# Kernel optimization log

Measured on AMD Instinct MI355X. Metric: run time of the kernel, lower is better.

Reference implementation:

```python
import jax, jax.numpy as jnp
import numpy as np

B, N, C, H = 16, 577, 384, 6
ONE_DIM = 24
RPD = 2 * ONE_DIM - 1  # 47
NUM_CLS = 1
HEAD_DIM = C // H
SCALE = HEAD_DIM ** -0.5


def _build_rel_pos_index():
    # Faithful to the torch loop: tmp[dy - y + off, dx - x + off] with
    # torch's negative-index wraparound -> modulo RPD.
    off = ONE_DIM // 2
    qy = np.repeat(np.arange(ONE_DIM), ONE_DIM)  # (Np,) y of each query patch
    qx = np.tile(np.arange(ONE_DIM), ONE_DIM)    # (Np,) x of each query patch
    ky, kx = qy, qx                              # key patches use same grid
    ry = (ky[None, :] - qy[:, None] + off) % RPD
    rx = (kx[None, :] - qx[:, None] + off) % RPD
    return jnp.asarray(ry * RPD + rx, dtype=jnp.int32)  # (Np, Np)


def setup_inputs() -> dict:
    key = jax.random.key(0)
    k = jax.random.split(key, 6)
    x = jax.random.normal(k[0], (B, N, C), dtype=jnp.float32)
    qkv_w = jax.random.normal(k[1], (3 * C, C), dtype=jnp.float32) * 0.02
    qkv_b = jnp.zeros((3 * C,), dtype=jnp.float32)
    proj_w = jax.random.normal(k[2], (C, C), dtype=jnp.float32) * 0.02
    proj_b = jnp.zeros((C,), dtype=jnp.float32)
    rel_pos = jax.random.normal(k[3], (H, RPD * RPD), dtype=jnp.float32) * 0.02
    mask = jax.random.randint(k[4], (B, N, N), 0, 2, dtype=jnp.int32)
    return {
        "x": x, "qkv_w": qkv_w, "qkv_b": qkv_b,
        "proj_w": proj_w, "proj_b": proj_b, "rel_pos": rel_pos,
        "rel_pos_index": _build_rel_pos_index(),
        "mask": mask, "patch_attn": 1,
    }


def reference(x, qkv_w, qkv_b, proj_w, proj_b, rel_pos, rel_pos_index, mask, patch_attn):
    # qkv projection: torch Linear -> x @ W^T + b
    qkv = x @ qkv_w.T + qkv_b                               # (B, N, 3C)
    qkv = qkv.reshape(B, N, 3, H, HEAD_DIM).transpose(2, 0, 3, 1, 4)
    q, k, v = qkv[0], qkv[1], qkv[2]                        # (B, H, N, hd)

    attn = jnp.einsum("bhqd,bhkd->bhqk", q, k) * SCALE      # (B, H, N, N)

    if patch_attn:
        # gather per-head relative-position bias for patch tokens
        bias = rel_pos[:, rel_pos_index]                    # (H, Np, Np)
        attn = attn.at[:, :, NUM_CLS:, NUM_CLS:].add(bias)

    neg = jnp.finfo(attn.dtype).min
    attn = jnp.where(mask[:, None, :, :] == 0, neg, attn)   # broadcast over heads

    attn = jax.nn.softmax(attn, axis=-1)
    out = jnp.einsum("bhqk,bhkd->bhqd", attn, v)            # (B, H, N, hd)
    out = out.transpose(0, 2, 1, 3).reshape(B, N, C)
    out = out @ proj_w.T + proj_b
    return out
```

## Files before the change

kernel.cpp:

```cpp
#include <hip/hip_runtime.h>
#include <float.h>
#include <math.h>

#define NB 16
#define NN 577
#define NC 384
#define NH 6
#define ND 64
#define RPD2 2209
#define MTOT 9232
#define MPAD 9344
#define SCALE_ 0.125f
#define NEGBIG -3.0e38f
#define BSTRIDE 580
#define NKPAD 640

typedef __attribute__((ext_vector_type(8))) short bf16x8;
typedef __attribute__((ext_vector_type(4))) float f32x4;
typedef unsigned short u16;

#define MFMA16(a, b, c) __builtin_amdgcn_mfma_f32_16x16x32_bf16(a, b, c, 0, 0, 0)

#define SQA 3932160ull
#define OFF_QH 0ull
#define OFF_QL SQA
#define OFF_KH (2ull * SQA)
#define OFF_KL (3ull * SQA)
#define OFF_VTH (4ull * SQA)
#define OFF_VTL (5ull * SQA)
#define OFF_XH (6ull * SQA)
#define OFF_XL (6ull * SQA + 3588096ull)
#define OFF_WQH (6ull * SQA + 2ull * 3588096ull)
#define OFF_WQL (OFF_WQH + 442368ull)
#define OFF_WPH (OFF_WQL + 442368ull)
#define OFF_WPL (OFF_WPH + 147456ull)
#define OFF_BT  (OFF_WPL + 147456ull)
#define OFF_PM  (OFF_BT + 2007960ull)

static __device__ __forceinline__ u16 f2bf(float f) {
  unsigned u = __float_as_uint(f);
  u += 0x7fff + ((u >> 16) & 1);
  return (u16)(u >> 16);
}
static __device__ __forceinline__ float bf2f(u16 h) {
  return __uint_as_float((unsigned)h << 16);
}
static __device__ __forceinline__ void split2(float v, u16& hi, u16& lo) {
  hi = f2bf(v);
  lo = f2bf(v - bf2f(hi));
}
static __device__ __forceinline__ void gload16(const void* g, void* l) {
  __builtin_amdgcn_global_load_lds(
      (const __attribute__((address_space(1))) void*)g,
      (__attribute__((address_space(3))) void*)l, 16, 0, 0);
}

__global__ __launch_bounds__(256) void prep_k(
    const float* __restrict__ x, const float* __restrict__ wq,
    const float* __restrict__ wp, u16* __restrict__ ws)
{
  const int q = blockIdx.x * 256 + threadIdx.x;
  float4 v = {0.f, 0.f, 0.f, 0.f};
  u16 *dh, *dl;
  if (q < 897024) {
    if (q < 886272) v = ((const float4*)x)[q];
    dh = ws + OFF_XH + 4ull * q;
    dl = ws + OFF_XL + 4ull * q;
  } else if (q < 1007616) {
    int t = q - 897024;
    v = ((const float4*)wq)[t];
    dh = ws + OFF_WQH + 4ull * t;
    dl = ws + OFF_WQL + 4ull * t;
  } else {
    int t = q - 1007616;
    v = ((const float4*)wp)[t];
    dh = ws + OFF_WPH + 4ull * t;
    dl = ws + OFF_WPL + 4ull * t;
  }
  ushort4 hh, ll;
  split2(v.x, hh.x, ll.x);
  split2(v.y, hh.y, ll.y);
  split2(v.z, hh.z, ll.z);
  split2(v.w, hh.w, ll.w);
  *(ushort4*)dh = hh;
  *(ushort4*)dl = ll;
}

__global__ __launch_bounds__(256, 3) void qkv_mfma_k(
    const u16* __restrict__ Xh, const u16* __restrict__ Xl,
    const u16* __restrict__ Wh, const u16* __restrict__ Wl,
    const float* __restrict__ bias, const int* __restrict__ mask,
    const float* __restrict__ rel_pos, const int* __restrict__ rel_idx,
    const int* __restrict__ patch, u16* __restrict__ ws)
{
  __shared__ u16 LB[16384];

  const int bid = blockIdx.x;
  const int tid = threadIdx.x;

  if (bid >= 1314) {
    if (bid < 3622) {
      unsigned* pm = (unsigned*)(ws + OFF_PM);
      const int pbid = bid - 1314;
      const int wid = (pbid * 256 + tid) >> 6;
      const int lane = tid & 63;
      if (wid >= MTOT) return;
      const int* mr = mask + (size_t)wid * NN;
#pragma unroll
      for (int c = 0; c < 10; ++c) {
        int k = c * 64 + lane;
        int v = (k < NN) ? mr[k] : 0;
        unsigned long long bal = __ballot(v != 0);
        if (lane == 0) pm[wid * 20 + 2 * c] = (unsigned)bal;
        if (lane == 1) pm[wid * 20 + 2 * c + 1] = (unsigned)(bal >> 32);
      }
    } else {
      const int f = bid - 3622;
      const int q = f % NN, h = f / NN;
      const int pa = *patch;
      u16* row = ws + OFF_BT + ((size_t)h * NN + q) * BSTRIDE;
      for (int kk = tid; kk < BSTRIDE; kk += 256) {
        float v = 0.f;
        if (pa && q >= 1 && kk >= 1 && kk < NN)
          v = rel_pos[h * RPD2 + rel_idx[(q - 1) * 576 + (kk - 1)]];
        row[kk] = f2bf(v);
      }
    }
    return;
  }

#define pASH(bf) (LB + (bf) * 4096)
#define pASL(bf) (LB + 8192 + (bf) * 4096)

  const int w = tid >> 6, l = tid & 63, lq = l & 15, lg = l >> 4;
  const int wm = (w >> 1) * 64, wn = (w & 1) * 32;

  const int o = bid;
  const int xcd = o & 7, rank = o >> 3;
  const int wg = (xcd < 2) ? (xcd * 165 + rank)
                           : (330 + (xcd - 2) * 164 + rank);
  const int mb = (wg / 18) * 128;
  const int rbi = wg % 18;
  const int rb = rbi * 64;
  const int r0 = rb + wn;
  const int soff = (l >> 2) * 384 + (l & 3) * 8;

#define STAGE_A(k0_, bf_)                                                    \
  {                                                                          \
    _Pragma("unroll")                                                        \
    for (int j = 0; j < 2; ++j) {                                            \
      const int tr = 32 * w + 16 * j;                                        \
      const size_t ga = (size_t)(mb + tr) * 384 + (k0_) + soff;              \
      gload16(&Xh[ga], pASH(bf_) + tr * 32);                                 \
      gload16(&Xl[ga], pASL(bf_) + tr * 32);                                 \
    }                                                                        \
  }

  const size_t brow = (size_t)(r0 + lq) * 384 + 8 * lg;
#define BLOAD(k0_, BH_, BL_)                                                 \
  {                                                                          \
    _Pragma("unroll")                                                        \
    for (int nt = 0; nt < 2; ++nt) {                                         \
      BH_[nt] = *(const bf16x8*)&Wh[brow + (size_t)(16 * nt) * 384 + (k0_)]; \
      BL_[nt] = *(const bf16x8*)&Wl[brow + (size_t)(16 * nt) * 384 + (k0_)]; \
    }                                                                        \
  }

#define COMPUTE(bf_, BH_, BL_)                                               \
  {                                                                          \
    _Pragma("unroll")                                                        \
    for (int mt = 0; mt < 4; ++mt) {                                         \
      bf16x8 ah = *(const bf16x8*)(pASH(bf_) + (wm + 16 * mt + lq) * 32 + 8 * lg); \
      bf16x8 al = *(const bf16x8*)(pASL(bf_) + (wm + 16 * mt + lq) * 32 + 8 * lg); \
      _Pragma("unroll")                                                      \
      for (int nt = 0; nt < 2; ++nt) {                                       \
        acc[mt][nt] = MFMA16(ah, BH_[nt], acc[mt][nt]);                      \
        acc[mt][nt] = MFMA16(ah, BL_[nt], acc[mt][nt]);                      \
        acc[mt][nt] = MFMA16(al, BH_[nt], acc[mt][nt]);                      \
      }                                                                      \
    }                                                                        \
  }

  bf16x8 bh2[2][2], bl2[2][2];
  STAGE_A(0, 0);
  BLOAD(0, bh2[0], bl2[0]);

  f32x4 acc[4][2];
#pragma unroll
  for (int nt = 0; nt < 2; ++nt) {
    float bv = bias[r0 + 16 * nt + lq];
#pragma unroll
    for (int mt = 0; mt < 4; ++mt) acc[mt][nt] = (f32x4){bv, bv, bv, bv};
  }

#pragma unroll
  for (int k = 0; k < 12; ++k) {
    const int cur = k & 1;
    asm volatile("s_waitcnt vmcnt(4)" ::: "memory");
    __builtin_amdgcn_sched_barrier(0);
    __builtin_amdgcn_s_barrier();
    __builtin_amdgcn_sched_barrier(0);
    asm volatile("s_waitcnt vmcnt(0)" ::: "memory");
    __builtin_amdgcn_sched_barrier(0);
    if (k < 11) {
      STAGE_A(32 * (k + 1), cur ^ 1);
      BLOAD(32 * (k + 1), bh2[cur ^ 1], bl2[cur ^ 1]);
    }
    COMPUTE(cur, bh2[cur], bl2[cur]);
  }

#undef COMPUTE
#undef BLOAD
#undef STAGE_A

  const int comp = rbi / 6;
  const int h = rbi % 6;

  if (comp != 2) {
#pragma unroll
    for (int mt = 0; mt < 4; ++mt)
#pragma unroll
      for (int r = 0; r < 4; ++r) {
        int m = mb + wm + 16 * mt + 4 * lg + r;
        if (m >= MTOT) continue;
        int bb = m / NN, nn = m - bb * NN;
        int bh = bb * NH + h;
#pragma unroll
        for (int nt = 0; nt < 2; ++nt) {
          int d = wn + 16 * nt + lq;
          float v = acc[mt][nt][r];
          u16 hi, lo;
          if (comp == 0) {
            v *= SCALE_;
            split2(v, hi, lo);
            size_t a = ((size_t)bh * NKPAD + nn) * 64 + d;
            ws[OFF_QH + a] = hi;
            ws[OFF_QL + a] = lo;
          } else {
            split2(v, hi, lo);
            size_t a = ((size_t)bh * NKPAD + nn) * 64 + d;
            ws[OFF_KH + a] = hi;
            ws[OFF_KL + a] = lo;
          }
        }
      }
  } else {
    __syncthreads();
    u16* scr = LB + w * 2304;
    const int mlane = mb + wm + l;
    const bool mv = mlane < MTOT;
    int bb = 0, nn = 0;
    if (mv) { bb = mlane / NN; nn = mlane - bb * NN; }
    const size_t vbase = (((size_t)(bb * NH + h) * 64 + wn)) * NKPAD + nn;

    for (int part = 0; part < 2; ++part) {
      u16* dst = ws + (part ? OFF_VTL : OFF_VTH);
#pragma unroll
      for (int nt = 0; nt < 2; ++nt)
#pragma unroll
        for (int mt = 0; mt < 4; ++mt) {
          ushort4 pk;
          u16 hi, lo;
          split2(acc[mt][nt][0], hi, lo); pk.x = part ? lo : hi;
          split2(acc[mt][nt][1], hi, lo); pk.y = part ? lo : hi;
          split2(acc[mt][nt][2], hi, lo); pk.z = part ? lo : hi;
          split2(acc[mt][nt][3], hi, lo); pk.w = part ? lo : hi;
          *(ushort4*)&scr[(16 * nt + lq) * 72 + 16 * mt + 4 * lg] = pk;
        }
      if (mv) {
        for (int i = 0; i < 32; ++i)
          dst[vbase + (size_t)i * NKPAD] = scr[i * 72 + l];
      }
    }
  }
#undef pASH
#undef pASL
}

__global__ __launch_bounds__(256, 2) void attn_k(
    const u16* __restrict__ Qh, const u16* __restrict__ Ql,
    const u16* __restrict__ Kh, const u16* __restrict__ Kl,
    const u16* __restrict__ Vth, const u16* __restrict__ Vtl,
    const u16* __restrict__ btbl, const unsigned* __restrict__ pm,
    u16* __restrict__ Oh, u16* __restrict__ Ol)
{
  __shared__ u16 Kth[2][4096], Ktl[2][4096];
  __shared__ u16 Vsh[2][4096], Vsl[2][4096];
  __shared__ u16 Ph[4][2048];

  const int tid = threadIdx.x;
  const int w = tid >> 6, l = tid & 63, lq = l & 15, lg = l >> 4;
  const int q0 = blockIdx.x * 128;
  const int h = blockIdx.y, b = blockIdx.z;
  const int bh = b * NH + h;
  const int qr0 = q0 + 32 * w + lq;
  const int qr1 = qr0 + 16;
  const int swz = (lq & 7) << 3;
  const int ln8 = l >> 3, lc8 = l & 7;
  const int koff = ln8 * 64 + ((lc8 ^ ln8) << 3);
  const int voff = ln8 * NKPAD + ((lc8 ^ ln8) << 3);

#define STAGE(ch, bf)                                                        \
  {                                                                          \
    const int kb_ = (ch) * 64;                                               \
    const size_t kgb = ((size_t)bh * NKPAD + kb_ + 16 * w) * 64 + koff;      \
    const size_t vgb = ((size_t)bh * 64 + 16 * w) * NKPAD + kb_ + voff;      \
    gload16(&Kh[kgb],              &Kth[bf][(16 * w) * 64]);                 \
    gload16(&Kh[kgb + 512],        &Kth[bf][(16 * w + 8) * 64]);             \
    gload16(&Kl[kgb],              &Ktl[bf][(16 * w) * 64]);                 \
    gload16(&Kl[kgb + 512],        &Ktl[bf][(16 * w + 8) * 64]);             \
    gload16(&Vth[vgb],             &Vsh[bf][(16 * w) * 64]);                 \
    gload16(&Vth[vgb + 8 * NKPAD], &Vsh[bf][(16 * w + 8) * 64]);             \
    gload16(&Vtl[vgb],             &Vsl[bf][(16 * w) * 64]);                 \
    gload16(&Vtl[vgb + 8 * NKPAD], &Vsl[bf][(16 * w + 8) * 64]);             \
  }

  STAGE(0, 0);

  const size_t qb0 = ((size_t)bh * NKPAD + qr0) * 64 + 8 * lg;
  const size_t qb1 = ((size_t)bh * NKPAD + qr1) * 64 + 8 * lg;
  bf16x8 q0h[2], q0l[2], q1h[2], q1l[2];
  q0h[0] = *(const bf16x8*)&Qh[qb0];
  q0h[1] = *(const bf16x8*)&Qh[qb0 + 32];
  q0l[0] = *(const bf16x8*)&Ql[qb0];
  q0l[1] = *(const bf16x8*)&Ql[qb0 + 32];
  q1h[0] = *(const bf16x8*)&Qh[qb1];
  q1h[1] = *(const bf16x8*)&Qh[qb1 + 32];
  q1l[0] = *(const bf16x8*)&Ql[qb1];
  q1l[1] = *(const bf16x8*)&Ql[qb1 + 32];

  const int gq0 = (qr0 < NN) ? qr0 : NN - 1;
  const int gq1 = (qr1 < NN) ? qr1 : NN - 1;
  const bool qv0 = qr0 < NN, qv1 = qr1 < NN;
  const unsigned* pmrow0 = pm + ((size_t)b * NN + gq0) * 20;
  const unsigned* pmrow1 = pm + ((size_t)b * NN + gq1) * 20;
  const size_t brow0 = ((size_t)h * NN + gq0) * BSTRIDE;
  const size_t brow1 = ((size_t)h * NN + gq1) * BSTRIDE;

  uint2 cM0, cM1, nM0, nM1;
  uint2 cB0[4], cB1[4], nB0[4], nB1[4];
  cM0 = *(const uint2*)&pmrow0[0];
  cM1 = *(const uint2*)&pmrow1[0];
#pragma unroll
  for (int t = 0; t < 4; ++t) {
    int kkb = 16 * t + 4 * lg;
    cB0[t] = (qv0 && kkb <= 576) ? *(const uint2*)&btbl[brow0 + kkb]
                                 : make_uint2(0u, 0u);
    cB1[t] = (qv1 && kkb <= 576) ? *(const uint2*)&btbl[brow1 + kkb]
                                 : make_uint2(0u, 0u);
  }

  float m_reg0 = NEGBIG, l_reg0 = 0.f;
  float m_reg1 = NEGBIG, l_reg1 = 0.f;
  f32x4 accO0[4] = {}, accO1[4] = {};

  for (int ch = 0; ch < 10; ++ch) {
    const int bf = ch & 1;
    __syncthreads();
    if (ch < 9) {
      nM0 = *(const uint2*)&pmrow0[2 * (ch + 1)];
      nM1 = *(const uint2*)&pmrow1[2 * (ch + 1)];
      const int kb2 = (ch + 1) * 64;
#pragma unroll
      for (int t = 0; t < 4; ++t) {
        int kkb = kb2 + 16 * t + 4 * lg;
        nB0[t] = (qv0 && kkb <= 576) ? *(const uint2*)&btbl[brow0 + kkb]
                                     : make_uint2(0u, 0u);
        nB1[t] = (qv1 && kkb <= 576) ? *(const uint2*)&btbl[brow1 + kkb]
                                     : make_uint2(0u, 0u);
      }
      STAGE(ch + 1, bf ^ 1);
    }

    unsigned long long m64_0 = (unsigned long long)cM0.x |
                               ((unsigned long long)cM0.y << 32);
    unsigned long long m64_1 = (unsigned long long)cM1.x |
                               ((unsigned long long)cM1.y << 32);

    float sv0[4][4], sv1[4][4];
    __builtin_amdgcn_s_setprio(1);
#pragma unroll
    for (int t = 0; t < 4; ++t) {
      f32x4 a0, a1;
      a0[0] = bf2f((u16)(cB0[t].x & 0xffff));
      a0[1] = bf2f((u16)(cB0[t].x >> 16));
      a0[2] = bf2f((u16)(cB0[t].y & 0xffff));
      a0[3] = bf2f((u16)(cB0[t].y >> 16));
      a1[0] = bf2f((u16)(cB1[t].x & 0xffff));
      a1[1] = bf2f((u16)(cB1[t].x >> 16));
      a1[2] = bf2f((u16)(cB1[t].y & 0xffff));
      a1[3] = bf2f((u16)(cB1[t].y >> 16));
      const int ar = (16 * t + lq) * 64;
#pragma unroll
      for (int ks = 0; ks < 2; ++ks) {
        const int c = (8 * lg + 32 * ks) ^ swz;
        bf16x8 ah = *(const bf16x8*)&Kth[bf][ar + c];
        bf16x8 al = *(const bf16x8*)&Ktl[bf][ar + c];
        a0 = MFMA16(ah, q0h[ks], a0);
        a0 = MFMA16(ah, q0l[ks], a0);
        a0 = MFMA16(al, q0h[ks], a0);
        a1 = MFMA16(ah, q1h[ks], a1);
        a1 = MFMA16(ah, q1l[ks], a1);
        a1 = MFMA16(al, q1h[ks], a1);
      }
#pragma unroll
      for (int r = 0; r < 4; ++r) { sv0[t][r] = a0[r]; sv1[t][r] = a1[r]; }
    }
    __builtin_amdgcn_s_setprio(0);

    {
      float cmax = NEGBIG;
#pragma unroll
      for (int t = 0; t < 4; ++t)
#pragma unroll
        for (int r = 0; r < 4; ++r) {
          int kl = 16 * t + 4 * lg + r;
          float s = ((m64_0 >> kl) & 1ull) ? sv0[t][r] : NEGBIG;
          sv0[t][r] = s;
          cmax = fmaxf(cmax, s);
        }
      cmax = fmaxf(cmax, __shfl_xor(cmax, 16));
      cmax = fmaxf(cmax, __shfl_xor(cmax, 32));
      float m_new = fmaxf(m_reg0, cmax);
      float fx = __expf(m_reg0 - m_new);
      float csum = 0.f;
#pragma unroll
      for (int t = 0; t < 4; ++t) {
        float e0 = __expf(sv0[t][0] - m_new);
        float e1 = __expf(sv0[t][1] - m_new);
        float e2 = __expf(sv0[t][2] - m_new);
        float e3 = __expf(sv0[t][3] - m_new);
        csum += e0 + e1 + e2 + e3;
        ushort4 ph;
        ph.x = f2bf(e0); ph.y = f2bf(e1); ph.z = f2bf(e2); ph.w = f2bf(e3);
        *(ushort4*)&Ph[w][lq * 64 + ((16 * t + 4 * lg) ^ swz)] = ph;
      }
      csum += __shfl_xor(csum, 16);
      csum += __shfl_xor(csum, 32);
      l_reg0 = l_reg0 * fx + csum;
      m_reg0 = m_new;
      float fxr[4];
#pragma unroll
      for (int r = 0; r < 4; ++r) fxr[r] = __shfl(fx, 4 * lg + r);
#pragma unroll
      for (int t = 0; t < 4; ++t) {
        accO0[t][0] *= fxr[0]; accO0[t][1] *= fxr[1];
        accO0[t][2] *= fxr[2]; accO0[t][3] *= fxr[3];
      }
    }
    {
      float cmax = NEGBIG;
#pragma unroll
      for (int t = 0; t < 4; ++t)
#pragma unroll
        for (int r = 0; r < 4; ++r) {
          int kl = 16 * t + 4 * lg + r;
          float s = ((m64_1 >> kl) & 1ull) ? sv1[t][r] : NEGBIG;
          sv1[t][r] = s;
          cmax = fmaxf(cmax, s);
        }
      cmax = fmaxf(cmax, __shfl_xor(cmax, 16));
      cmax = fmaxf(cmax, __shfl_xor(cmax, 32));
      float m_new = fmaxf(m_reg1, cmax);
      float fx = __expf(m_reg1 - m_new);
      float csum = 0.f;
#pragma unroll
      for (int t = 0; t < 4; ++t) {
        float e0 = __expf(sv1[t][0] - m_new);
        float e1 = __expf(sv1[t][1] - m_new);
        float e2 = __expf(sv1[t][2] - m_new);
        float e3 = __expf(sv1[t][3] - m_new);
        csum += e0 + e1 + e2 + e3;
        ushort4 ph;
        ph.x = f2bf(e0); ph.y = f2bf(e1); ph.z = f2bf(e2); ph.w = f2bf(e3);
        *(ushort4*)&Ph[w][(16 + lq) * 64 + ((16 * t + 4 * lg) ^ swz)] = ph;
      }
      csum += __shfl_xor(csum, 16);
      csum += __shfl_xor(csum, 32);
      l_reg1 = l_reg1 * fx + csum;
      m_reg1 = m_new;
      float fxr[4];
#pragma unroll
      for (int r = 0; r < 4; ++r) fxr[r] = __shfl(fx, 4 * lg + r);
#pragma unroll
      for (int t = 0; t < 4; ++t) {
        accO1[t][0] *= fxr[0]; accO1[t][1] *= fxr[1];
        accO1[t][2] *= fxr[2]; accO1[t][3] *= fxr[3];
      }
    }

    bf16x8 pa0[2], pa1[2];
#pragma unroll
    for (int ks = 0; ks < 2; ++ks) {
      int c = (8 * lg + 32 * ks) ^ swz;
      pa0[ks] = *(const bf16x8*)&Ph[w][lq * 64 + c];
      pa1[ks] = *(const bf16x8*)&Ph[w][(16 + lq) * 64 + c];
    }

    __builtin_amdgcn_s_setprio(1);
#pragma unroll
    for (int t = 0; t < 4; ++t) {
      const int vr = (16 * t + lq) * 64;
#pragma unroll
      for (int ks = 0; ks < 2; ++ks) {
        const int c = (8 * lg + 32 * ks) ^ swz;
        bf16x8 vh = *(const bf16x8*)&Vsh[bf][vr + c];
        bf16x8 vl = *(const bf16x8*)&Vsl[bf][vr + c];
        accO0[t] = MFMA16(pa0[ks], vh, accO0[t]);
        accO0[t] = MFMA16(pa0[ks], vl, accO0[t]);
        accO1[t] = MFMA16(pa1[ks], vh, accO1[t]);
        accO1[t] = MFMA16(pa1[ks], vl, accO1[t]);
      }
    }
    __builtin_amdgcn_s_setprio(0);

    if (ch < 9) {
      cM0 = nM0; cM1 = nM1;
#pragma unroll
      for (int t = 0; t < 4; ++t) { cB0[t] = nB0[t]; cB1[t] = nB1[t]; }
    }
  }
#undef STAGE

  float il0 = 1.f / l_reg0;
  float il1 = 1.f / l_reg1;
  float ilr0[4], ilr1[4];
#pragma unroll
  for (int r = 0; r < 4; ++r) {
    ilr0[r] = __shfl(il0, 4 * lg + r);
    ilr1[r] = __shfl(il1, 4 * lg + r);
  }
#pragma unroll
  for (int t = 0; t < 4; ++t)
#pragma unroll
    for (int r = 0; r < 4; ++r) {
      int g0 = q0 + 32 * w + 4 * lg + r;
      if (g0 < NN) {
        float v = accO0[t][r] * ilr0[r];
        u16 hi, lo;
        split2(v, hi, lo);
        size_t a = ((size_t)b * NN + g0) * NC + h * 64 + 16 * t + lq;
        Oh[a] = hi;
        Ol[a] = lo;
      }
      int g1 = g0 + 16;
      if (g1 < NN) {
        float v = accO1[t][r] * ilr1[r];
        u16 hi, lo;
        split2(v, hi, lo);
        size_t a = ((size_t)b * NN + g1) * NC + h * 64 + 16 * t + lq;
        Oh[a] = hi;
        Ol[a] = lo;
      }
    }
}

__global__ __launch_bounds__(256, 3) void proj_mfma_k(
    const u16* __restrict__ Ah, const u16* __restrict__ Al,
    const u16* __restrict__ Wh, const u16* __restrict__ Wl,
    const float* __restrict__ bias, float* __restrict__ out)
{
  __shared__ u16 Ash[2][2048], Asl[2][2048];

  const int tid = threadIdx.x;
  const int w = tid >> 6, l = tid & 63, lq = l & 15, lg = l >> 4;
  const int wm = (w >> 1) * 32, wn = (w & 1) * 32;
  const int mb = blockIdx.x * 64;
  const int rb = blockIdx.y * 64;
  const int r0 = rb + wn;
  const int soff = (l >> 2) * 384 + (l & 3) * 8;

#define STAGE_A(k0_, bf_)                                                    \
  {                                                                          \
    const int tr = 16 * w;                                                   \
    const size_t ga = (size_t)(mb + tr) * 384 + (k0_) + soff;                \
    gload16(&Ah[ga], &Ash[bf_][tr * 32]);                                    \
    gload16(&Al[ga], &Asl[bf_][tr * 32]);                                    \
  }

  const size_t brow = (size_t)(r0 + lq) * 384 + 8 * lg;
#define BLOAD(k0_, BH_, BL_)                                                 \
  {                                                                          \
    _Pragma("unroll")                                                        \
    for (int nt = 0; nt < 2; ++nt) {                                         \
      BH_[nt] = *(const bf16x8*)&Wh[brow + (size_t)(16 * nt) * 384 + (k0_)]; \
      BL_[nt] = *(const bf16x8*)&Wl[brow + (size_t)(16 * nt) * 384 + (k0_)]; \
    }                                                                        \
  }

#define COMPUTE(bf_, BH_, BL_)                                               \
  {                                                                          \
    _Pragma("unroll")                                                        \
    for (int mt = 0; mt < 2; ++mt) {                                         \
      bf16x8 ah = *(const bf16x8*)&Ash[bf_][(wm + 16 * mt + lq) * 32 + 8 * lg]; \
      bf16x8 al = *(const bf16x8*)&Asl[bf_][(wm + 16 * mt + lq) * 32 + 8 * lg]; \
      _Pragma("unroll")                                                      \
      for (int nt = 0; nt < 2; ++nt) {                                       \
        acc[mt][nt] = MFMA16(ah, BH_[nt], acc[mt][nt]);                      \
        acc[mt][nt] = MFMA16(ah, BL_[nt], acc[mt][nt]);                      \
        acc[mt][nt] = MFMA16(al, BH_[nt], acc[mt][nt]);                      \
      }                                                                      \
    }                                                                        \
  }

  bf16x8 bh2[2][2], bl2[2][2];
  STAGE_A(0, 0);
  BLOAD(0, bh2[0], bl2[0]);

  f32x4 acc[2][2];
#pragma unroll
  for (int nt = 0; nt < 2; ++nt) {
    float bv = bias[r0 + 16 * nt + lq];
#pragma unroll
    for (int mt = 0; mt < 2; ++mt) acc[mt][nt] = (f32x4){bv, bv, bv, bv};
  }

#pragma unroll
  for (int k = 0; k < 12; ++k) {
    const int cur = k & 1;
    asm volatile("s_waitcnt vmcnt(4)" ::: "memory");
    __builtin_amdgcn_sched_barrier(0);
    __builtin_amdgcn_s_barrier();
    __builtin_amdgcn_sched_barrier(0);
    asm volatile("s_waitcnt vmcnt(0)" ::: "memory");
    __builtin_amdgcn_sched_barrier(0);
    if (k < 11) {
      STAGE_A(32 * (k + 1), cur ^ 1);
      BLOAD(32 * (k + 1), bh2[cur ^ 1], bl2[cur ^ 1]);
    }
    COMPUTE(cur, bh2[cur], bl2[cur]);
  }

#undef COMPUTE
#undef BLOAD
#undef STAGE_A

#pragma unroll
  for (int mt = 0; mt < 2; ++mt)
#pragma unroll
    for (int r = 0; r < 4; ++r) {
      int m = mb + wm + 16 * mt + 4 * lg + r;
      if (m >= MTOT) continue;
#pragma unroll
      for (int nt = 0; nt < 2; ++nt)
        out[(size_t)m * NC + r0 + 16 * nt + lq] = acc[mt][nt][r];
    }
}

extern "C" void kernel_launch(void* const* d_in, const int* in_sizes, int n_in,
                              void* d_out, int out_size, void* d_ws, size_t ws_size,
                              hipStream_t stream) {
  const float* x       = (const float*)d_in[0];
  const float* qkv_w   = (const float*)d_in[1];
  const float* qkv_b   = (const float*)d_in[2];
  const float* proj_w  = (const float*)d_in[3];
  const float* proj_b  = (const float*)d_in[4];
  const float* rel_pos = (const float*)d_in[5];
  const int*   rel_idx = (const int*)d_in[6];
  const int*   mask    = (const int*)d_in[7];
  const int*   patch   = (const int*)d_in[8];
  float* out = (float*)d_out;
  u16* W16 = (u16*)d_ws;

  unsigned* pmp = (unsigned*)(W16 + OFF_PM);
  u16* btblp = W16 + OFF_BT;

  prep_k<<<4080, 256, 0, stream>>>(x, qkv_w, proj_w, W16);
  qkv_mfma_k<<<7084, 256, 0, stream>>>(
      W16 + OFF_XH, W16 + OFF_XL, W16 + OFF_WQH, W16 + OFF_WQL, qkv_b,
      mask, rel_pos, rel_idx, patch, W16);
  attn_k<<<dim3(5, NH, NB), 256, 0, stream>>>(
      W16 + OFF_QH, W16 + OFF_QL, W16 + OFF_KH, W16 + OFF_KL,
      W16 + OFF_VTH, W16 + OFF_VTL, btblp, pmp,
      W16 + OFF_XH, W16 + OFF_XL);
  proj_mfma_k<<<dim3(146, 6), 256, 0, stream>>>(
      W16 + OFF_XH, W16 + OFF_XL, W16 + OFF_WPH, W16 + OFF_WPL, proj_b, out);
}
```

Before: 148.3 us.

## Triple-buffer LDS A-tiles in qkv and proj GEMMs for deeper prefetch

Expands the LDS A-operand staging from double to triple buffering in both the QKV and projection GEMM kernels. A tiles are now issued two k-steps ahead and the vmcnt waits are relaxed, so the loop no longer drains all outstanding loads before each compute step. The goal is to hide global-to-LDS latency behind MFMA work. The cost is more LDS per block (which may limit occupancy at launch_bounds 3) and fragile hand-counted vmcnt values.

```diff
diff --git a/kernel.cpp b/kernel.cpp
--- a/kernel.cpp
+++ b/kernel.cpp
@@ -54,6 +54,7 @@
       (const __attribute__((address_space(1))) void*)g,
       (__attribute__((address_space(3))) void*)l, 16, 0, 0);
 }
+#define SB0() __builtin_amdgcn_sched_barrier(0)
 
 __global__ __launch_bounds__(256) void prep_k(
     const float* __restrict__ x, const float* __restrict__ wq,
@@ -93,7 +94,7 @@
     const float* __restrict__ rel_pos, const int* __restrict__ rel_idx,
     const int* __restrict__ patch, u16* __restrict__ ws)
 {
-  __shared__ u16 LB[16384];
+  __shared__ u16 LB[24576];
 
   const int bid = blockIdx.x;
   const int tid = threadIdx.x;
@@ -130,7 +131,7 @@
   }
 
 #define pASH(bf) (LB + (bf) * 4096)
-#define pASL(bf) (LB + 8192 + (bf) * 4096)
+#define pASL(bf) (LB + 12288 + (bf) * 4096)
 
   const int w = tid >> 6, l = tid & 63, lq = l & 15, lg = l >> 4;
   const int wm = (w >> 1) * 64, wn = (w & 1) * 32;
@@ -184,6 +185,7 @@
   bf16x8 bh2[2][2], bl2[2][2];
   STAGE_A(0, 0);
   BLOAD(0, bh2[0], bl2[0]);
+  STAGE_A(32, 1);
 
   f32x4 acc[4][2];
 #pragma unroll
@@ -195,18 +197,19 @@
 
 #pragma unroll
   for (int k = 0; k < 12; ++k) {
-    const int cur = k & 1;
-    asm volatile("s_waitcnt vmcnt(4)" ::: "memory");
-    __builtin_amdgcn_sched_barrier(0);
+    if (k < 11) { asm volatile("s_waitcnt vmcnt(8)" ::: "memory"); }
+    else        { asm volatile("s_waitcnt vmcnt(4)" ::: "memory"); }
+    SB0();
     __builtin_amdgcn_s_barrier();
-    __builtin_amdgcn_sched_barrier(0);
-    asm volatile("s_waitcnt vmcnt(0)" ::: "memory");
-    __builtin_amdgcn_sched_barrier(0);
-    if (k < 11) {
-      STAGE_A(32 * (k + 1), cur ^ 1);
-      BLOAD(32 * (k + 1), bh2[cur ^ 1], bl2[cur ^ 1]);
-    }
-    COMPUTE(cur, bh2[cur], bl2[cur]);
+    SB0();
+    if (k < 11) BLOAD(32 * (k + 1), bh2[(k + 1) & 1], bl2[(k + 1) & 1]);
+    if (k < 10) STAGE_A(32 * (k + 2), (k + 2) % 3);
+    SB0();
+    if (k < 10)      { asm volatile("s_waitcnt vmcnt(12)" ::: "memory"); }
+    else if (k == 10){ asm volatile("s_waitcnt vmcnt(8)"  ::: "memory"); }
+    else             { asm volatile("s_waitcnt vmcnt(0)"  ::: "memory"); }
+    SB0();
+    COMPUTE(k % 3, bh2[k & 1], bl2[k & 1]);
   }
 
 #undef COMPUTE
@@ -560,7 +563,7 @@
     const u16* __restrict__ Wh, const u16* __restrict__ Wl,
     const float* __restrict__ bias, float* __restrict__ out)
 {
-  __shared__ u16 Ash[2][2048], Asl[2][2048];
+  __shared__ u16 Ash[3][2048], Asl[3][2048];
 
   const int tid = threadIdx.x;
   const int w = tid >> 6, l = tid & 63, lq = l & 15, lg = l >> 4;
@@ -606,6 +609,7 @@
   bf16x8 bh2[2][2], bl2[2][2];
   STAGE_A(0, 0);
   BLOAD(0, bh2[0], bl2[0]);
+  STAGE_A(32, 1);
 
   f32x4 acc[2][2];
 #pragma unroll
@@ -617,18 +621,19 @@
 
 #pragma unroll
   for (int k = 0; k < 12; ++k) {
-    const int cur = k & 1;
-    asm volatile("s_waitcnt vmcnt(4)" ::: "memory");
-    __builtin_amdgcn_sched_barrier(0);
+    if (k < 11) { asm volatile("s_waitcnt vmcnt(6)" ::: "memory"); }
+    else        { asm volatile("s_waitcnt vmcnt(4)" ::: "memory"); }
+    SB0();
     __builtin_amdgcn_s_barrier();
-    __builtin_amdgcn_sched_barrier(0);
-    asm volatile("s_waitcnt vmcnt(0)" ::: "memory");
-    __builtin_amdgcn_sched_barrier(0);
-    if (k < 11) {
-      STAGE_A(32 * (k + 1), cur ^ 1);
-      BLOAD(32 * (k + 1), bh2[cur ^ 1], bl2[cur ^ 1]);
-    }
-    COMPUTE(cur, bh2[cur], bl2[cur]);
+    SB0();
+    if (k < 11) BLOAD(32 * (k + 1), bh2[(k + 1) & 1], bl2[(k + 1) & 1]);
+    if (k < 10) STAGE_A(32 * (k + 2), (k + 2) % 3);
+    SB0();
+    if (k < 10)      { asm volatile("s_waitcnt vmcnt(8)" ::: "memory"); }
+    else if (k == 10){ asm volatile("s_waitcnt vmcnt(6)" ::: "memory"); }
+    else             { asm volatile("s_waitcnt vmcnt(0)" ::: "memory"); }
+    SB0();
+    COMPUTE(k % 3, bh2[k & 1], bl2[k & 1]);
   }
 
 #undef COMPUTE
```

Result: slower. 155.8 us (+5.1%).
